# Kernel optimization log

Hardware: AMD Instinct MI355X
Metric: run time of the kernel (lower is better)

Reference implementation:

```python
import jax, jax.numpy as jnp
import numpy as np

B, N, D = 2, 2048, 1024
H, DH = 16, 64
DI = 4096
EPS = 1e-5
NEG_SLOPE = 0.01  # F.leaky_relu default


def _ln(x, g, b):
    mu = jnp.mean(x, axis=-1, keepdims=True)
    var = jnp.mean((x - mu) ** 2, axis=-1, keepdims=True)
    return (x - mu) * jax.lax.rsqrt(var + EPS) * g + b


def setup_inputs() -> dict:
    key = jax.random.key(0)
    ks = jax.random.split(key, 10)
    s = 0.02
    return {
        "Z": jax.random.normal(ks[0], (B, N, D), jnp.float32),
        "new_mask": jax.random.normal(ks[1], (B, N, N), jnp.float32),
        "mask": jax.random.uniform(ks[2], (B, N, N), jnp.float32),
        "ln1_g": jnp.ones((D,), jnp.float32),
        "ln1_b": jnp.zeros((D,), jnp.float32),
        "qkv_w": jax.random.normal(ks[3], (3 * D, D), jnp.float32) * s,
        "qkv_b": jnp.zeros((3 * D,), jnp.float32),
        "o_w": jax.random.normal(ks[4], (D, H * DH), jnp.float32) * s,
        "ln2_g": jnp.ones((D,), jnp.float32),
        "ln2_b": jnp.zeros((D,), jnp.float32),
        "p1_w": jax.random.normal(ks[5], (DI, D), jnp.float32) * s,
        "p1_b": jnp.zeros((DI,), jnp.float32),
        "p2_w": jax.random.normal(ks[6], (D, DI), jnp.float32) * s,
        "p2_b": jnp.zeros((D,), jnp.float32),
    }


def reference(Z, new_mask, mask, ln1_g, ln1_b, qkv_w, qkv_b, o_w, ln2_g, ln2_b, p1_w, p1_b, p2_w, p2_b):
    inp = Z
    Zn = _ln(Z, ln1_g, ln1_b)
    qkv = (Zn @ qkv_w.T + qkv_b).reshape(B, N, H, 3 * DH)
    # torch chunk order in the source: V, Q, K
    V, Q, K = jnp.split(qkv, 3, axis=3)  # each [B,N,H,DH]
    # scores: einsum('bnij,bmij->binm') == [B,H,N,N]
    W = jnp.einsum("bnhd,bmhd->bhnm", Q, K) / np.sqrt(DH) + new_mask[:, None]
    A = jax.nn.softmax(W, axis=3) * mask[:, None]
    attn = jnp.einsum("bhnm,bmhd->bnhd", A, V).reshape(B, N, D)
    attn = jnp.where(attn >= 0, attn, NEG_SLOPE * attn) @ o_w.T  # leaky_relu then o_net (no bias)
    Z1 = attn + inp
    Zn2 = _ln(Z1, ln2_g, ln2_b)
    h = jax.nn.relu(Zn2 @ p1_w.T + p1_b)
    return h @ p2_w.T + p2_b + Z1
```

## Files before the change

kernel.cpp:

```cpp
#include <hip/hip_runtime.h>

typedef unsigned short u16;
typedef __attribute__((ext_vector_type(8))) short bf16x8;
typedef __attribute__((ext_vector_type(2))) float f32x2;
typedef __attribute__((ext_vector_type(4))) float f32x4;
typedef __attribute__((ext_vector_type(16))) float f32x16;
typedef __attribute__((ext_vector_type(4))) unsigned u32x4;

#define DEV static __device__ __forceinline__

DEV u16 f2bf(float f) {
    unsigned u = __float_as_uint(f);
    u += 0x7FFFu + ((u >> 16) & 1u);
    return (u16)(u >> 16);
}

DEV float uaf(unsigned u) { return __uint_as_float(u); }

typedef const __attribute__((address_space(1))) void* gas1_t;
typedef __attribute__((address_space(3))) void* gas3_t;

DEV void gl_lds16(const u16* g, u16* l) {
    __builtin_amdgcn_global_load_lds((gas1_t)g, (gas3_t)l, 16, 0, 0);
}

DEV unsigned cvtpk_bf16(float a, float b) {
    unsigned r;
    asm("v_cvt_pk_bf16_f32 %0, %1, %2" : "=v"(r) : "v"(a), "v"(b));
    return r;
}

DEV int sw8(int row, int chunk) { return row * 64 + ((chunk ^ (row & 7)) << 3); }

__global__ __launch_bounds__(256) void prep_all(const float* __restrict__ qkv_w,
                                                const float* __restrict__ o_w,
                                                const float* __restrict__ p1_w,
                                                const float* __restrict__ p2_w,
                                                const float* __restrict__ qkv_b,
                                                const float* __restrict__ nm,
                                                const float* __restrict__ pm,
                                                u16* __restrict__ qkvW,
                                                u16* __restrict__ oW,
                                                u16* __restrict__ p1W,
                                                u16* __restrict__ p2W,
                                                float* __restrict__ pbias,
                                                unsigned* __restrict__ Mp) {
    __shared__ uint4 Ls[512];
    const int bid = blockIdx.x, t = threadIdx.x;
    if (bid < 3072) {
        int i = bid * 256 + t;
        int orow = i >> 8, cc = i & 255;
        int region = orow >> 10, rem = orow & 1023, h = rem >> 6, tt = rem & 63;
        int srow = h * 192 + region * 64 + tt;
        float4 v = ((const float4*)qkv_w)[srow * 256 + cc];
        ushort4 o;
        o.x = f2bf(v.x); o.y = f2bf(v.y); o.z = f2bf(v.z); o.w = f2bf(v.w);
        ((ushort4*)qkvW)[i] = o;
    } else if (bid < 4096) {
        int i = (bid - 3072) * 256 + t;
        float4 v = ((const float4*)o_w)[i];
        ushort4 o;
        o.x = f2bf(v.x); o.y = f2bf(v.y); o.z = f2bf(v.z); o.w = f2bf(v.w);
        ((ushort4*)oW)[i] = o;
    } else if (bid < 8192) {
        int i = (bid - 4096) * 256 + t;
        float4 v = ((const float4*)p1_w)[i];
        ushort4 o;
        o.x = f2bf(v.x); o.y = f2bf(v.y); o.z = f2bf(v.z); o.w = f2bf(v.w);
        ((ushort4*)p1W)[i] = o;
    } else if (bid < 12288) {
        int i = (bid - 8192) * 256 + t;
        float4 v = ((const float4*)p2_w)[i];
        ushort4 o;
        o.x = f2bf(v.x); o.y = f2bf(v.y); o.z = f2bf(v.z); o.w = f2bf(v.w);
        ((ushort4*)p2W)[i] = o;
    } else if (bid < 16384) {
        const int idx = bid - 12288;
        const int bb = idx >> 11, r2 = idx & 2047;
        const int mt = r2 >> 5, nt = r2 & 31;
        const int n0 = nt * 64;
        const int n = t >> 2;
        const int mq0 = (t & 3) * 2;
        const size_t fbase = (size_t)bb * 1048576 + (size_t)(n0 + n) * 512 + mt * 8 + mq0;
        const float4 a0 = ((const float4*)nm)[fbase];
        const float4 a1 = ((const float4*)nm)[fbase + 1];
        const float4 b0 = ((const float4*)pm)[fbase];
        const float4 b1 = ((const float4*)pm)[fbase + 1];
        uint4 o0, o1;
        o0.x = ((unsigned)f2bf(b0.x) << 16) | f2bf(a0.x * 1.4426950f);
        o0.y = ((unsigned)f2bf(b0.y) << 16) | f2bf(a0.y * 1.4426950f);
        o0.z = ((unsigned)f2bf(b0.z) << 16) | f2bf(a0.z * 1.4426950f);
        o0.w = ((unsigned)f2bf(b0.w) << 16) | f2bf(a0.w * 1.4426950f);
        o1.x = ((unsigned)f2bf(b1.x) << 16) | f2bf(a1.x * 1.4426950f);
        o1.y = ((unsigned)f2bf(b1.y) << 16) | f2bf(a1.y * 1.4426950f);
        o1.z = ((unsigned)f2bf(b1.z) << 16) | f2bf(a1.z * 1.4426950f);
        o1.w = ((unsigned)f2bf(b1.w) << 16) | f2bf(a1.w * 1.4426950f);
        const int c = mq0 >> 1;
        Ls[c * 128 + n * 2 + 0] = o0;
        Ls[c * 128 + n * 2 + 1] = o1;
        __syncthreads();
        const int wc = t >> 6, j = t & 63;
        const size_t obase = (((size_t)(bb * 64 + mt) * 4) + wc) * 4096 + (size_t)n0 * 2;
        ((uint4*)Mp)[obase + j] = Ls[wc * 128 + j];
        ((uint4*)Mp)[obase + 64 + j] = Ls[wc * 128 + 64 + j];
    } else {
#pragma unroll
        for (int k = 0; k < 12; k++) {
            int i = k * 256 + t;
            int region = i >> 10, rem = i & 1023, h = rem >> 6, tt = rem & 63;
            pbias[i] = qkv_b[h * 192 + region * 64 + tt];
        }
    }
}

__global__ __launch_bounds__(256) void ln_bf16(const float* __restrict__ x,
                                               const float* __restrict__ gam,
                                               const float* __restrict__ bet,
                                               u16* __restrict__ y) {
    const int row = blockIdx.x;
    const int t = threadIdx.x;
    const float4 v = ((const float4*)(x + (size_t)row * 1024))[t];
    float s = v.x + v.y + v.z + v.w;
    float ss = v.x * v.x + v.y * v.y + v.z * v.z + v.w * v.w;
#pragma unroll
    for (int o = 1; o < 64; o <<= 1) {
        s += __shfl_xor(s, o);
        ss += __shfl_xor(ss, o);
    }
    __shared__ float rs[4], rss[4];
    const int wave = t >> 6, lane = t & 63;
    if (lane == 0) { rs[wave] = s; rss[wave] = ss; }
    __syncthreads();
    const float tot = rs[0] + rs[1] + rs[2] + rs[3];
    const float totss = rss[0] + rss[1] + rss[2] + rss[3];
    const float mu = tot * (1.0f / 1024.0f);
    const float var = totss * (1.0f / 1024.0f) - mu * mu;
    const float rstd = rsqrtf(var + 1e-5f);
    const float4 g4 = ((const float4*)gam)[t];
    const float4 b4 = ((const float4*)bet)[t];
    ushort4 o;
    o.x = f2bf((v.x - mu) * rstd * g4.x + b4.x);
    o.y = f2bf((v.y - mu) * rstd * g4.y + b4.y);
    o.z = f2bf((v.z - mu) * rstd * g4.z + b4.z);
    o.w = f2bf((v.w - mu) * rstd * g4.w + b4.w);
    ((ushort4*)(y + (size_t)row * 1024))[t] = o;
}

__global__ __launch_bounds__(256) void ln2_comb4(const float* __restrict__ p0,
                                                 const float* __restrict__ p1,
                                                 const float* __restrict__ p2,
                                                 const float* __restrict__ p3,
                                                 const float* __restrict__ Z,
                                                 const float* __restrict__ gam,
                                                 const float* __restrict__ bet,
                                                 float* __restrict__ Z1,
                                                 u16* __restrict__ y) {
    const int row = blockIdx.x;
    const int t = threadIdx.x;
    const size_t off = (size_t)row * 256 + t;
    const float4 a = ((const float4*)p0)[off];
    const float4 c = ((const float4*)p1)[off];
    const float4 d = ((const float4*)p2)[off];
    const float4 e = ((const float4*)p3)[off];
    const float4 z = ((const float4*)Z)[off];
    float4 v;
    v.x = a.x + c.x + d.x + e.x + z.x;
    v.y = a.y + c.y + d.y + e.y + z.y;
    v.z = a.z + c.z + d.z + e.z + z.z;
    v.w = a.w + c.w + d.w + e.w + z.w;
    ((float4*)Z1)[off] = v;
    float s = v.x + v.y + v.z + v.w;
    float ss = v.x * v.x + v.y * v.y + v.z * v.z + v.w * v.w;
#pragma unroll
    for (int o = 1; o < 64; o <<= 1) {
        s += __shfl_xor(s, o);
        ss += __shfl_xor(ss, o);
    }
    __shared__ float rs[4], rss[4];
    const int wave = t >> 6, lane = t & 63;
    if (lane == 0) { rs[wave] = s; rss[wave] = ss; }
    __syncthreads();
    const float tot = rs[0] + rs[1] + rs[2] + rs[3];
    const float totss = rss[0] + rss[1] + rss[2] + rss[3];
    const float mu = tot * (1.0f / 1024.0f);
    const float var = totss * (1.0f / 1024.0f) - mu * mu;
    const float rstd = rsqrtf(var + 1e-5f);
    const float4 g4 = ((const float4*)gam)[t];
    const float4 b4 = ((const float4*)bet)[t];
    ushort4 o;
    o.x = f2bf((v.x - mu) * rstd * g4.x + b4.x);
    o.y = f2bf((v.y - mu) * rstd * g4.y + b4.y);
    o.z = f2bf((v.z - mu) * rstd * g4.z + b4.z);
    o.w = f2bf((v.w - mu) * rstd * g4.w + b4.w);
    ((ushort4*)(y + (size_t)row * 1024))[t] = o;
}

__global__ __launch_bounds__(256) void out_comb(const float* __restrict__ p0,
                                                const float* __restrict__ p1,
                                                const float* __restrict__ bias,
                                                const float* __restrict__ Z1,
                                                float* __restrict__ out) {
    int i = blockIdx.x * 256 + threadIdx.x;
    float4 a = ((const float4*)p0)[i];
    float4 c = ((const float4*)p1)[i];
    float4 z = ((const float4*)Z1)[i];
    float4 b = ((const float4*)bias)[i & 255];
    float4 o;
    o.x = a.x + c.x + z.x + b.x; o.y = a.y + c.y + z.y + b.y;
    o.z = a.z + c.z + z.z + b.z; o.w = a.w + c.w + z.w + b.w;
    ((float4*)out)[i] = o;
}

template <int EPI>
__global__ __launch_bounds__(256, 3) void gemm_bt(const u16* __restrict__ A,
                                                  const u16* __restrict__ Bt,
                                                  const float* __restrict__ bias,
                                                  void* __restrict__ out0,
                                                  void* __restrict__ out1,
                                                  void* __restrict__ out2,
                                                  int M, int N, int K, int ldk) {
    __shared__ __align__(16) u16 As[128 * 32];
    __shared__ __align__(16) u16 Bs[128 * 32];
    const int tid = threadIdx.x;
    const int wave = tid >> 6, lane = tid & 63;
    const int lhi = lane >> 4, llo = lane & 15;
    const int bx = blockIdx.x, by = blockIdx.y;
    const int kz = blockIdx.z * K;

    const int arow = wave * 32 + (lane >> 2);
    const int acol = (lane & 3) * 8;
    const u16* gA = A + (size_t)(by * 128 + arow) * ldk + kz + acol;
    const u16* gB = Bt + (size_t)(bx * 128 + arow) * ldk + kz + acol;
    u16* lA = As + wave * 1024 + lane * 8;
    u16* lB = Bs + wave * 1024 + lane * 8;

    const int wr = wave >> 1, wc = wave & 1;
    const f32x4 zero = {0.f, 0.f, 0.f, 0.f};
    f32x4 acc[4][4];
#pragma unroll
    for (int i = 0; i < 4; i++)
#pragma unroll
        for (int j = 0; j < 4; j++) acc[i][j] = zero;

    for (int k0 = 0; k0 < K; k0 += 32) {
        __syncthreads();
        gl_lds16(gA, lA);
        gl_lds16(gA + 16 * (size_t)ldk, lA + 512);
        gl_lds16(gB, lB);
        gl_lds16(gB + 16 * (size_t)ldk, lB + 512);
        gA += 32; gB += 32;
        __syncthreads();
        bf16x8 af[4], bfr[4];
#pragma unroll
        for (int i = 0; i < 4; i++)
            af[i] = *(const bf16x8*)(As + (wr * 64 + i * 16 + llo) * 32 + lhi * 8);
#pragma unroll
        for (int j = 0; j < 4; j++)
            bfr[j] = *(const bf16x8*)(Bs + (wc * 64 + j * 16 + llo) * 32 + lhi * 8);
#pragma unroll
        for (int i = 0; i < 4; i++)
#pragma unroll
            for (int j = 0; j < 4; j++)
                acc[i][j] = __builtin_amdgcn_mfma_f32_16x16x32_bf16(af[i], bfr[j], acc[i][j], 0, 0, 0);
    }

    const int rbase = by * 128 + wr * 64 + lhi * 4;
    const int cbase = bx * 128 + wc * 64 + llo;
    float* pout = nullptr;
    if constexpr (EPI == 4) {
        pout = (blockIdx.z < 2) ? ((float*)out0 + (size_t)blockIdx.z * M * N)
                                : ((float*)out1 + (size_t)(blockIdx.z - 2) * M * N);
    }
#pragma unroll
    for (int i = 0; i < 4; i++) {
#pragma unroll
        for (int j = 0; j < 4; j++) {
#pragma unroll
            for (int r = 0; r < 4; r++) {
                const int row = rbase + i * 16 + r;
                const int col = cbase + j * 16;
                float v = acc[i][j][r];
                if constexpr (EPI == 0) {
                    v += bias[col];
                    const int region = col >> 10;
                    const int c = col & 1023;
                    const int b = row >> 11, n = row & 2047;
                    if (region == 0) {
                        ((float*)out0)[(size_t)row * 1024 + c] = v;
                    } else {
                        const int h = c >> 6, t = c & 63;
                        u16* dst = (region == 1) ? (u16*)out1 : (u16*)out2;
                        dst[(((size_t)(b * 16 + h)) * 2048 + n) * 64 + t] = f2bf(v);
                    }
                } else if constexpr (EPI == 2) {
                    v += bias[col];
                    v = v > 0.f ? v : 0.f;
                    ((u16*)out0)[(size_t)row * N + col] = f2bf(v);
                } else {
                    pout[(size_t)row * N + col] = v;
                }
            }
        }
    }
}

__global__ __launch_bounds__(256) void vtrans(const float* __restrict__ Vsc,
                                              u16* __restrict__ Vt) {
    __shared__ u16 Ts[64 * 72];
    const int nt = blockIdx.x;
    const int bh = blockIdx.y;
    const int b = bh >> 4, h = bh & 15;
    const int t = threadIdx.x;
    const int n0 = nt * 64;
    const int nr = t >> 2;
    const int dq = (t & 3) * 16;
    const float* src = Vsc + ((size_t)(b * 2048 + n0 + nr)) * 1024 + h * 64 + dq;
    float4 v0 = ((const float4*)src)[0];
    float4 v1 = ((const float4*)src)[1];
    float4 v2 = ((const float4*)src)[2];
    float4 v3 = ((const float4*)src)[3];
    u16* c0 = Ts + nr;
    c0[(dq + 0) * 72]  = f2bf(v0.x); c0[(dq + 1) * 72]  = f2bf(v0.y);
    c0[(dq + 2) * 72]  = f2bf(v0.z); c0[(dq + 3) * 72]  = f2bf(v0.w);
    c0[(dq + 4) * 72]  = f2bf(v1.x); c0[(dq + 5) * 72]  = f2bf(v1.y);
    c0[(dq + 6) * 72]  = f2bf(v1.z); c0[(dq + 7) * 72]  = f2bf(v1.w);
    c0[(dq + 8) * 72]  = f2bf(v2.x); c0[(dq + 9) * 72]  = f2bf(v2.y);
    c0[(dq + 10) * 72] = f2bf(v2.z); c0[(dq + 11) * 72] = f2bf(v2.w);
    c0[(dq + 12) * 72] = f2bf(v3.x); c0[(dq + 13) * 72] = f2bf(v3.y);
    c0[(dq + 14) * 72] = f2bf(v3.z); c0[(dq + 15) * 72] = f2bf(v3.w);
    __syncthreads();
    const int d = t >> 2, n8 = (t & 3) * 16;
    u16* dstrow = Vt + ((size_t)bh * 64 + d) * 2048 + n0;
#pragma unroll
    for (int w = 0; w < 4; w++) {
        const int gi = (n8 >> 2) + w;
        const int g5 = gi & 7, blk = gi >> 3;
        const int pg = (g5 & 4) | ((g5 & 1) << 1) | ((g5 >> 1) & 1);
        *(uint2*)(dstrow + blk * 32 + pg * 4) = *(const uint2*)(Ts + d * 72 + n8 + w * 4);
    }
}

__global__ __launch_bounds__(256, 4) void attn_fused8(const u16* __restrict__ Qg,
                                                      const u16* __restrict__ Kg,
                                                      const u16* __restrict__ Vtg,
                                                      const unsigned* __restrict__ Mp,
                                                      u16* __restrict__ attnL) {
    __shared__ __align__(16) u16 Ks[2][64 * 64];
    __shared__ __align__(16) u16 Vs[2][64 * 64];
    __shared__ float lsh[2][32], lsh2[2][32];
    const int tid = threadIdx.x, wave = tid >> 6, lane = tid & 63;
    const int qh = wave & 1, wm = wave >> 1;
    const int hi = lane >> 5, l31 = lane & 31;
    const int pid = blockIdx.x;
    const int seq = pid >> 3;
    const int hh = seq & 15;
    const int g = (pid & 7) + (seq >> 4) * 8;
    const int b = g >> 5, qt = g & 31;
    const int bh = b * 16 + hh;
    const int q0 = qt * 64;

    const int l3 = lane >> 3, l7 = lane & 7;
    const int swcol = (l7 ^ l3) << 3;
    const int srow = wave * 16 + l3;
    const u16* kp = Kg + ((size_t)bh * 2048 + srow) * 64 + swcol;
    const u16* vp = Vtg + ((size_t)bh * 64 + srow) * 2048 + swcol;
    u16* lKa = Ks[0] + wave * 1024 + lane * 8;
    u16* lKb = Ks[1] + wave * 1024 + lane * 8;
    u16* lVa = Vs[0] + wave * 1024 + lane * 8;
    u16* lVb = Vs[1] + wave * 1024 + lane * 8;

#define STAGE(LK, LV) do { \
        gl_lds16(kp, LK); gl_lds16(kp + 512, (LK) + 512); \
        gl_lds16(vp, LV); gl_lds16(vp + 16384, (LV) + 512); \
        kp += 4096; vp += 64; } while (0)

    STAGE(lKa, lVa);
    const int qrow = q0 + qh * 32 + l31;
    const u16* qptr = Qg + ((size_t)bh * 2048 + qrow) * 64 + hi * 8;
    bf16x8 qf[4];
#pragma unroll
    for (int ks = 0; ks < 4; ks++) qf[ks] = *(const bf16x8*)(qptr + ks * 16);

    const uint4* mp = (const uint4*)Mp + (size_t)(b * 64 + wm) * 16384
                                       + (size_t)qrow * 2 + hi;

    const f32x16 z16 = {0.f,0.f,0.f,0.f,0.f,0.f,0.f,0.f,0.f,0.f,0.f,0.f,0.f,0.f,0.f,0.f};
    f32x16 accO[2];
    accO[0] = z16; accO[1] = z16;
    f32x2 lsv = {0.f, 0.f};
    const float CS = 0.125f * 1.4426950f;
    const f32x2 csv = {CS, CS};
    __syncthreads();

#define QUAD(M, q) { \
        f32x2 nm0 = {uaf(M.x << 16), uaf(M.y << 16)}; \
        f32x2 nm1 = {uaf(M.z << 16), uaf(M.w << 16)}; \
        const f32x2 sa = {sacc[q], sacc[q + 1]}; \
        const f32x2 sb = {sacc[q + 2], sacc[q + 3]}; \
        nm0 += sa * csv; nm1 += sb * csv; \
        f32x2 e0 = {__builtin_amdgcn_exp2f(nm0.x), __builtin_amdgcn_exp2f(nm0.y)}; \
        f32x2 e1 = {__builtin_amdgcn_exp2f(nm1.x), __builtin_amdgcn_exp2f(nm1.y)}; \
        lsv += e0; lsv += e1; \
        const f32x2 pm0 = {uaf(M.x & 0xFFFF0000u), uaf(M.y & 0xFFFF0000u)}; \
        const f32x2 pm1 = {uaf(M.z & 0xFFFF0000u), uaf(M.w & 0xFFFF0000u)}; \
        e0 *= pm0; e1 *= pm1; \
        wpk[(q) / 2] = cvtpk_bf16(e0.x, e0.y); \
        wpk[(q) / 2 + 1] = cvtpk_bf16(e1.x, e1.y); }

#define ITER(KSB, VSB, LK, LV, DO_STAGE) do { \
        const uint4 M0 = mp[0], M1 = mp[4096], M2 = mp[8192], M3 = mp[12288]; \
        mp += 32768; \
        if (DO_STAGE) STAGE(LK, LV); \
        f32x16 sacc = z16; \
        __builtin_amdgcn_s_setprio(1); \
        _Pragma("unroll") \
        for (int ks = 0; ks < 4; ks++) { \
            const bf16x8 kf = *(const bf16x8*)((KSB) + sw8(wm * 32 + l31, ks * 2 + hi)); \
            sacc = __builtin_amdgcn_mfma_f32_32x32x16_bf16(kf, qf[ks], sacc, 0, 0, 0); \
        } \
        __builtin_amdgcn_s_setprio(0); \
        unsigned wpk[8]; \
        QUAD(M0, 0) QUAD(M1, 4) QUAD(M2, 8) QUAD(M3, 12) \
        const u32x4 fa0v = {wpk[0], wpk[1], wpk[2], wpk[3]}; \
        const u32x4 fa1v = {wpk[4], wpk[5], wpk[6], wpk[7]}; \
        const bf16x8 pa0 = __builtin_bit_cast(bf16x8, fa0v); \
        const bf16x8 pa1 = __builtin_bit_cast(bf16x8, fa1v); \
        __builtin_amdgcn_s_setprio(1); \
        _Pragma("unroll") \
        for (int dh = 0; dh < 2; dh++) { \
            const bf16x8 vf0 = *(const bf16x8*)((VSB) + sw8(dh * 32 + l31, wm * 4 + hi)); \
            accO[dh] = __builtin_amdgcn_mfma_f32_32x32x16_bf16(pa0, vf0, accO[dh], 0, 0, 0); \
            const bf16x8 vf1 = *(const bf16x8*)((VSB) + sw8(dh * 32 + l31, wm * 4 + 2 + hi)); \
            accO[dh] = __builtin_amdgcn_mfma_f32_32x32x16_bf16(pa1, vf1, accO[dh], 0, 0, 0); \
        } \
        __builtin_amdgcn_s_setprio(0); \
        __syncthreads(); } while (0)

    for (int tt = 0; tt < 16; tt++) {
        ITER(Ks[0], Vs[0], lKb, lVb, true);
        ITER(Ks[1], Vs[1], lKa, lVa, (tt < 15));
    }
#undef ITER
#undef QUAD
#undef STAGE

    const float lsum = lsv.x + lsv.y;
    const float lsum2 = lsum + __shfl_xor(lsum, 32);
    float* cb = (float*)&Ks[0][0];
    const int slot = qh * 64 + lane;
    const int s7 = slot & 7;
    if (wm == 1) {
        float* dst = cb + (size_t)slot * 32;
#pragma unroll
        for (int dh = 0; dh < 2; dh++)
#pragma unroll
            for (int c = 0; c < 4; c++) {
                const f32x4 v = {accO[dh][c * 4 + 0], accO[dh][c * 4 + 1],
                                 accO[dh][c * 4 + 2], accO[dh][c * 4 + 3]};
                *(f32x4*)(dst + (((dh * 4 + c) ^ s7) << 2)) = v;
            }
        if (lane < 32) lsh[qh][lane] = lsum2;
    }
    __syncthreads();
    if (wm == 0) {
        const float* src = cb + (size_t)slot * 32;
        const float lt = lsum2 + lsh[qh][l31];
#pragma unroll
        for (int dh = 0; dh < 2; dh++)
#pragma unroll
            for (int c = 0; c < 4; c++) {
                const f32x4 v = *(const f32x4*)(src + (((dh * 4 + c) ^ s7) << 2));
                accO[dh][c * 4 + 0] += v.x;
                accO[dh][c * 4 + 1] += v.y;
                accO[dh][c * 4 + 2] += v.z;
                accO[dh][c * 4 + 3] += v.w;
            }
        if (lane < 32) lsh2[qh][lane] = 1.0f / lt;
    }
    __syncthreads();
    if (wm == 0) {
#pragma unroll
        for (int r = 0; r < 16; r++) {
            const int ql = (r & 3) + 8 * (r >> 2) + 4 * hi;
            const float linv = lsh2[qh][ql];
            const int qg = q0 + qh * 32 + ql;
#pragma unroll
            for (int dh = 0; dh < 2; dh++) {
                float v = accO[dh][r] * linv;
                v = v >= 0.f ? v : 0.01f * v;
                attnL[((size_t)b * 2048 + qg) * 1024 + hh * 64 + dh * 32 + l31] = f2bf(v);
            }
        }
    }
}

extern "C" void kernel_launch(void* const* d_in, const int* in_sizes, int n_in,
                              void* d_out, int out_size, void* d_ws, size_t ws_size,
                              hipStream_t stream) {
    const float* Z     = (const float*)d_in[0];
    const float* nmask = (const float*)d_in[1];
    const float* pmask = (const float*)d_in[2];
    const float* ln1_g = (const float*)d_in[3];
    const float* ln1_b = (const float*)d_in[4];
    const float* qkv_w = (const float*)d_in[5];
    const float* qkv_b = (const float*)d_in[6];
    const float* o_w   = (const float*)d_in[7];
    const float* ln2_g = (const float*)d_in[8];
    const float* ln2_b = (const float*)d_in[9];
    const float* p1_w  = (const float*)d_in[10];
    const float* p1_b  = (const float*)d_in[11];
    const float* p2_w  = (const float*)d_in[12];
    const float* p2_b  = (const float*)d_in[13];
    float* out = (float*)d_out;

    char* w = (char*)d_ws;
    auto take = [&](size_t bytes) -> char* {
        char* p = w;
        w += (bytes + 255) & ~(size_t)255;
        return p;
    };
    u16* qkvW   = (u16*)take((size_t)3072 * 1024 * 2);
    u16* oW     = (u16*)take((size_t)1024 * 1024 * 2);
    u16* p1W    = (u16*)take((size_t)4096 * 1024 * 2);
    u16* p2W    = (u16*)take((size_t)1024 * 4096 * 2);
    u16* Zn     = (u16*)take((size_t)4096 * 1024 * 2);
    u16* Qb     = (u16*)take((size_t)32 * 2048 * 64 * 2);
    u16* Kb     = (u16*)take((size_t)32 * 2048 * 64 * 2);
    u16* Vt     = (u16*)take((size_t)32 * 64 * 2048 * 2);
    u16* attnL  = (u16*)take((size_t)4096 * 1024 * 2);
    float* Z1   = (float*)take((size_t)4096 * 1024 * 4);
    u16* hbuf   = (u16*)take((size_t)4096 * 4096 * 2);
    unsigned* Mp = (unsigned*)take((size_t)2 * 2048 * 2048 * 4);
    float* pbias = (float*)take((size_t)3072 * 4);
    float* Vsc    = (float*)hbuf;
    float* part01 = (float*)Mp;
    float* part23 = (float*)hbuf;

    prep_all<<<dim3(16385), 256, 0, stream>>>(qkv_w, o_w, p1_w, p2_w, qkv_b, nmask, pmask,
                                              qkvW, oW, p1W, p2W, pbias, Mp);
    ln_bf16<<<dim3(4096), 256, 0, stream>>>(Z, ln1_g, ln1_b, Zn);
    gemm_bt<0><<<dim3(24, 32), 256, 0, stream>>>(Zn, qkvW, pbias, Vsc, Qb, Kb, 4096, 3072, 1024, 1024);
    vtrans<<<dim3(32, 32), 256, 0, stream>>>(Vsc, Vt);
    attn_fused8<<<dim3(1024), 256, 0, stream>>>(Qb, Kb, Vt, Mp, attnL);
    gemm_bt<4><<<dim3(8, 32, 4), 256, 0, stream>>>(attnL, oW, nullptr, part01, part23, nullptr,
                                                   4096, 1024, 256, 1024);
    ln2_comb4<<<dim3(4096), 256, 0, stream>>>(part01, part01 + (size_t)4096 * 1024,
                                              part23, part23 + (size_t)4096 * 1024,
                                              Z, ln2_g, ln2_b, Z1, Zn);
    gemm_bt<2><<<dim3(32, 32), 256, 0, stream>>>(Zn, p1W, p1_b, hbuf, nullptr, nullptr,
                                                 4096, 4096, 1024, 1024);
    gemm_bt<4><<<dim3(8, 32, 2), 256, 0, stream>>>(hbuf, p2W, nullptr, part01, nullptr, nullptr,
                                                   4096, 1024, 2048, 4096);
    out_comb<<<dim3(4096), 256, 0, stream>>>(part01, part01 + (size_t)4096 * 1024, p2_b, Z1, out);
}
```

Measured before the change: 437.0 us.

## Double-buffer GEMM LDS tiles, swizzle LDS layout, and remap block order

The bf16 GEMM now keeps two LDS buffers per operand, so the global-to-LDS load of the next K tile is issued before the MFMA work on the current tile, with one barrier per tile instead of two. The LDS column layout is XOR-swizzled by row to cut bank conflicts on the fragment reads, and block indices are remapped into groups of eight to improve L2 reuse. MFMA sections raise wave priority with s_setprio. LDS use doubles, which may reduce occupancy under launch_bounds(256,3). The K loop advances two tiles per iteration, and the remap divides the grid by eight, so both assume K is a multiple of 64 and the block count a multiple of eight.

```diff
diff --git a/kernel.cpp b/kernel.cpp
--- a/kernel.cpp
+++ b/kernel.cpp
@@ -219,20 +219,30 @@
                                                   void* __restrict__ out1,
                                                   void* __restrict__ out2,
                                                   int M, int N, int K, int ldk) {
-    __shared__ __align__(16) u16 As[128 * 32];
-    __shared__ __align__(16) u16 Bs[128 * 32];
+    __shared__ __align__(16) u16 As[2][128 * 32];
+    __shared__ __align__(16) u16 Bs[2][128 * 32];
     const int tid = threadIdx.x;
     const int wave = tid >> 6, lane = tid & 63;
     const int lhi = lane >> 4, llo = lane & 15;
-    const int bx = blockIdx.x, by = blockIdx.y;
+    const int gx = gridDim.x;
+    const int bid = blockIdx.y * gx + blockIdx.x;
+    const int swz = (bid & 7) * ((gx * gridDim.y) >> 3) + (bid >> 3);
+    const int bx = swz % gx, by = swz / gx;
     const int kz = blockIdx.z * K;
 
     const int arow = wave * 32 + (lane >> 2);
-    const int acol = (lane & 3) * 8;
-    const u16* gA = A + (size_t)(by * 128 + arow) * ldk + kz + acol;
-    const u16* gB = Bt + (size_t)(bx * 128 + arow) * ldk + kz + acol;
-    u16* lA = As + wave * 1024 + lane * 8;
-    u16* lB = Bs + wave * 1024 + lane * 8;
+    const int asw = ((lane & 3) ^ ((lane >> 2) & 3)) << 3;
+    const u16* gA = A + (size_t)(by * 128 + arow) * ldk + kz + asw;
+    const u16* gB = Bt + (size_t)(bx * 128 + arow) * ldk + kz + asw;
+    u16* lA0 = As[0] + wave * 1024 + lane * 8;
+    u16* lA1 = As[1] + wave * 1024 + lane * 8;
+    u16* lB0 = Bs[0] + wave * 1024 + lane * 8;
+    u16* lB1 = Bs[1] + wave * 1024 + lane * 8;
+
+#define GSTAGE(LA, LB) do { \
+        gl_lds16(gA, LA); gl_lds16(gA + 16 * (size_t)ldk, (LA) + 512); \
+        gl_lds16(gB, LB); gl_lds16(gB + 16 * (size_t)ldk, (LB) + 512); \
+        gA += 32; gB += 32; } while (0)
 
     const int wr = wave >> 1, wc = wave & 1;
     const f32x4 zero = {0.f, 0.f, 0.f, 0.f};
@@ -242,27 +252,37 @@
 #pragma unroll
         for (int j = 0; j < 4; j++) acc[i][j] = zero;
 
-    for (int k0 = 0; k0 < K; k0 += 32) {
-        __syncthreads();
-        gl_lds16(gA, lA);
-        gl_lds16(gA + 16 * (size_t)ldk, lA + 512);
-        gl_lds16(gB, lB);
-        gl_lds16(gB + 16 * (size_t)ldk, lB + 512);
-        gA += 32; gB += 32;
-        __syncthreads();
-        bf16x8 af[4], bfr[4];
-#pragma unroll
-        for (int i = 0; i < 4; i++)
-            af[i] = *(const bf16x8*)(As + (wr * 64 + i * 16 + llo) * 32 + lhi * 8);
-#pragma unroll
-        for (int j = 0; j < 4; j++)
-            bfr[j] = *(const bf16x8*)(Bs + (wc * 64 + j * 16 + llo) * 32 + lhi * 8);
-#pragma unroll
-        for (int i = 0; i < 4; i++)
-#pragma unroll
-            for (int j = 0; j < 4; j++)
-                acc[i][j] = __builtin_amdgcn_mfma_f32_16x16x32_bf16(af[i], bfr[j], acc[i][j], 0, 0, 0);
-    }
+#define GCOMP(AB, BB) do { \
+        bf16x8 af[4], bfr[4]; \
+        _Pragma("unroll") \
+        for (int i = 0; i < 4; i++) { \
+            const int r = wr * 64 + i * 16 + llo; \
+            af[i] = *(const bf16x8*)((AB) + r * 32 + (((lhi ^ r) & 3) << 3)); \
+        } \
+        _Pragma("unroll") \
+        for (int j = 0; j < 4; j++) { \
+            const int r = wc * 64 + j * 16 + llo; \
+            bfr[j] = *(const bf16x8*)((BB) + r * 32 + (((lhi ^ r) & 3) << 3)); \
+        } \
+        __builtin_amdgcn_s_setprio(1); \
+        _Pragma("unroll") \
+        for (int i = 0; i < 4; i++) \
+            _Pragma("unroll") \
+            for (int j = 0; j < 4; j++) \
+                acc[i][j] = __builtin_amdgcn_mfma_f32_16x16x32_bf16(af[i], bfr[j], acc[i][j], 0, 0, 0); \
+        __builtin_amdgcn_s_setprio(0); \
+        __syncthreads(); } while (0)
+
+    GSTAGE(lA0, lB0);
+    __syncthreads();
+    for (int k0 = 0; k0 < K; k0 += 64) {
+        if (k0 + 32 < K) GSTAGE(lA1, lB1);
+        GCOMP(As[0], Bs[0]);
+        if (k0 + 64 < K) GSTAGE(lA0, lB0);
+        GCOMP(As[1], Bs[1]);
+    }
+#undef GCOMP
+#undef GSTAGE
 
     const int rbase = by * 128 + wr * 64 + lhi * 4;
     const int cbase = bx * 128 + wc * 64 + llo;
```

Result: faster. 423.0 us (-3.2%).
